# Performance work log

Hardware: AMD Instinct MI355X
Metric: run time of the kernel (lower is better)

Reference implementation:

```python
import jax, jax.numpy as jnp
import numpy as np

B, T, F, C = 16, 750, 4096, 20
R_ACT, R_BKG = 8, 8
KEEP = 0.3  # dropout p=0.7 -> keep prob 0.3, inverted dropout scaling


def setup_inputs() -> dict:
    key = jax.random.key(0)
    k1, k2, k3, k4 = jax.random.split(key, 4)
    x = jax.random.normal(k1, (B, T, F), jnp.float32)
    W_cls = jax.random.normal(k2, (C, F), jnp.float32) * 0.02  # 1x1 conv weight, no bias
    mask_cls = jax.random.bernoulli(k3, KEEP, (B, T, F)).astype(jnp.float32) / KEEP
    select_mask = jax.random.bernoulli(k4, KEEP, (B, T)).astype(jnp.float32) / KEEP
    return {"x": x, "W_cls": W_cls, "mask_cls": mask_cls, "select_mask": select_mask}


def reference(x, W_cls, mask_cls, select_mask):
    features = x  # CAS_Module passes raw input through as 'features'
    # dropout(p=0.7) then 1x1 conv classifier (no bias): (B,T,F)@(F,C)->(B,T,C)
    cas = jnp.einsum('btf,cf->btc', features * mask_cls, W_cls)

    k_act = T // R_ACT
    k_bkg = T // R_BKG

    mag = jnp.linalg.norm(features, axis=2)            # (B,T)
    mag_drop = mag * select_mask                        # dropout-masked magnitudes
    mag_rev = jnp.max(mag, axis=1, keepdims=True) - mag
    mag_rev_drop = mag_rev * select_mask

    _, idx_act = jax.lax.top_k(mag_drop, k_act)         # (B,k_act)
    _, idx_bkg = jax.lax.top_k(mag_rev_drop, k_bkg)     # (B,k_bkg)

    feat_act = jnp.take_along_axis(features, idx_act[:, :, None], axis=1)  # (B,k_act,F)
    feat_bkg = jnp.take_along_axis(features, idx_bkg[:, :, None], axis=1)  # (B,k_bkg,F)

    # per-class top-k over time of cas scores
    topk_scores, _ = jax.lax.top_k(jnp.transpose(cas, (0, 2, 1)), k_act)   # (B,C,k_act)
    score_act = jax.nn.softmax(jnp.mean(topk_scores, axis=2), axis=1)      # (B,C)

    cas_bkg = jnp.take_along_axis(cas, idx_bkg[:, :, None], axis=1)        # (B,k_bkg,C)
    score_bkg = jax.nn.softmax(jnp.mean(cas_bkg, axis=1), axis=1)          # (B,C)

    cas_softmax = jax.nn.softmax(cas, axis=2)                              # (B,T,C)

    return (score_act, score_bkg, feat_act, feat_bkg, features, cas_softmax)
```

## Files before the change

kernel.cpp:

```cpp
#include <hip/hip_runtime.h>

#define BB 16
#define TT 750
#define FF 4096
#define CC 20
#define K_ACT 93
#define K_BKG 93
#define NROWS (BB * TT)

__global__ __launch_bounds__(256) void k_main(
    const float* __restrict__ x, const float* __restrict__ w,
    const float* __restrict__ mask, float* __restrict__ features,
    float* __restrict__ cas_ws, double* __restrict__ mag2_ws)
{
    const int tid = threadIdx.x;
    const int row0 = blockIdx.x * 4;

    float acc[4][CC];
#pragma unroll
    for (int r = 0; r < 4; ++r)
#pragma unroll
        for (int c = 0; c < CC; ++c) acc[r][c] = 0.f;
    double mg[4] = {0.0, 0.0, 0.0, 0.0};

#pragma unroll
    for (int k = 0; k < 2; ++k) {
        const int fb = k * 2048 + tid * 8;
        float mk[4][8];
#pragma unroll
        for (int r = 0; r < 4; ++r) {
            const size_t off = (size_t)(row0 + r) * FF + fb;
            const float4 a0 = *(const float4*)(x + off);
            const float4 a1 = *(const float4*)(x + off + 4);
            const float4 m0 = *(const float4*)(mask + off);
            const float4 m1 = *(const float4*)(mask + off + 4);
            *(float4*)(features + off) = a0;
            *(float4*)(features + off + 4) = a1;
            mk[r][0] = a0.x * m0.x; mk[r][1] = a0.y * m0.y;
            mk[r][2] = a0.z * m0.z; mk[r][3] = a0.w * m0.w;
            mk[r][4] = a1.x * m1.x; mk[r][5] = a1.y * m1.y;
            mk[r][6] = a1.z * m1.z; mk[r][7] = a1.w * m1.w;
            mg[r] = fma((double)a0.x, (double)a0.x, mg[r]);
            mg[r] = fma((double)a0.y, (double)a0.y, mg[r]);
            mg[r] = fma((double)a0.z, (double)a0.z, mg[r]);
            mg[r] = fma((double)a0.w, (double)a0.w, mg[r]);
            mg[r] = fma((double)a1.x, (double)a1.x, mg[r]);
            mg[r] = fma((double)a1.y, (double)a1.y, mg[r]);
            mg[r] = fma((double)a1.z, (double)a1.z, mg[r]);
            mg[r] = fma((double)a1.w, (double)a1.w, mg[r]);
        }
#pragma unroll
        for (int c = 0; c < CC; ++c) {
            const float4 w0 = *(const float4*)(w + (size_t)c * FF + fb);
            const float4 w1 = *(const float4*)(w + (size_t)c * FF + fb + 4);
            float wf[8] = {w0.x, w0.y, w0.z, w0.w, w1.x, w1.y, w1.z, w1.w};
#pragma unroll
            for (int r = 0; r < 4; ++r)
#pragma unroll
                for (int j = 0; j < 8; ++j)
                    acc[r][c] = fmaf(mk[r][j], wf[j], acc[r][c]);
        }
    }

    __shared__ float red[CC][256];
    __shared__ float red2[CC][8];
    __shared__ double dred[256];
    __shared__ double dred2[8];

    for (int r = 0; r < 4; ++r) {
#pragma unroll
        for (int c = 0; c < CC; ++c) red[c][tid] = acc[r][c];
        dred[tid] = mg[r];
        __syncthreads();
        if (tid < 160) {
            const int c = tid >> 3, seg = tid & 7;
            const float4* p = (const float4*)&red[c][seg * 32];
            float s = 0.f;
#pragma unroll
            for (int i = 0; i < 8; ++i) { const float4 v = p[i]; s += (v.x + v.y) + (v.z + v.w); }
            red2[c][seg] = s;
        } else if (tid < 168) {
            const int seg = tid - 160;
            double s = 0.0;
#pragma unroll
            for (int i = 0; i < 32; ++i) s += dred[seg * 32 + i];
            dred2[seg] = s;
        }
        __syncthreads();
        if (tid < CC) {
            float s = 0.f;
#pragma unroll
            for (int i = 0; i < 8; ++i) s += red2[tid][i];
            cas_ws[(size_t)(row0 + r) * CC + tid] = s;
        } else if (tid == CC) {
            double s = 0.0;
#pragma unroll
            for (int i = 0; i < 8; ++i) s += dred2[i];
            mag2_ws[row0 + r] = s;
        }
        __syncthreads();
    }
}

__global__ __launch_bounds__(256) void k_topk(
    const double* __restrict__ mag2_ws, const float* __restrict__ smask,
    int* __restrict__ idxA, int* __restrict__ idxB)
{
    const int b = blockIdx.x;
    const int chunk = blockIdx.y;
    const int tid = threadIdx.x;

    __shared__ double m2[TT];
    __shared__ unsigned char alive[TT];
    __shared__ double mred[256];

    for (int t = tid; t < TT; t += 256) {
        m2[t] = mag2_ws[b * TT + t];
        alive[t] = (smask[b * TT + t] != 0.f);
    }
    __syncthreads();
    double lm = 0.0;
    for (int t = tid; t < TT; t += 256) lm = fmax(lm, m2[t]);
    mred[tid] = lm;
    __syncthreads();
    for (int s = 128; s > 0; s >>= 1) {
        if (tid < s) mred[tid] = fmax(mred[tid], mred[tid + s]);
        __syncthreads();
    }
    const double mx = mred[0];

    const int t = chunk * 250 + tid;
    if (tid < 250 && t < TT && alive[t]) {
        const double v = m2[t];
        const bool posB = v < mx;
        int rA = 0, rB = 0;
        for (int u = 0; u < TT; ++u) {
            if (!alive[u]) continue;
            const double wv = m2[u];
            if (wv > v || (wv == v && u < t)) ++rA;
            if (posB && wv < mx && (wv < v || (wv == v && u < t))) ++rB;
        }
        if (rA < K_ACT) idxA[b * K_ACT + rA] = t;
        if (posB && rB < K_BKG) idxB[b * K_BKG + rB] = t;
    }
}

__global__ __launch_bounds__(256) void k_gather(
    const float* __restrict__ x, const int* __restrict__ idxA,
    const int* __restrict__ idxB, float* __restrict__ featA,
    float* __restrict__ featB)
{
    int g = blockIdx.x;
    const int nA = BB * K_ACT;
    const bool isB = (g >= nA);
    if (isB) g -= nA;
    const int b = g / K_ACT;
    int t = (isB ? idxB : idxA)[g];
    t = min(max(t, 0), TT - 1);
    const float4* src = (const float4*)(x + (size_t)(b * TT + t) * FF);
    float4* dst = (float4*)((isB ? featB : featA) + (size_t)g * FF);
    for (int i = threadIdx.x; i < FF / 4; i += 256) dst[i] = src[i];
}

__global__ __launch_bounds__(256) void k_colmean(
    const float* __restrict__ cas_ws, float* __restrict__ meansA)
{
    const int b = blockIdx.x / CC;
    const int c = blockIdx.x % CC;
    const int tid = threadIdx.x;

    __shared__ float col[TT];
    __shared__ float pred[256];

    for (int t = tid; t < TT; t += 256) col[t] = cas_ws[(size_t)(b * TT + t) * CC + c];
    __syncthreads();

    float loc = 0.f;
    for (int t = tid; t < TT; t += 256) {
        const float v = col[t];
        int cnt = 0;
        for (int u = 0; u < TT; ++u) {
            const float wv = col[u];
            cnt += (wv > v) || (wv == v && u < t);
        }
        if (cnt < K_ACT) loc += v;
    }
    pred[tid] = loc;
    __syncthreads();
    for (int s = 128; s > 0; s >>= 1) {
        if (tid < s) pred[tid] += pred[tid + s];
        __syncthreads();
    }
    if (tid == 0) meansA[b * CC + c] = pred[0] / (float)K_ACT;
}

__global__ void k_scores(
    const float* __restrict__ cas_ws, const float* __restrict__ meansA,
    const int* __restrict__ idxB, float* __restrict__ score_act,
    float* __restrict__ score_bkg)
{
    const int b = blockIdx.x;
    const int tid = threadIdx.x;
    __shared__ float mB[CC];

    if (tid < CC) {
        float s = 0.f;
        for (int j = 0; j < K_BKG; ++j) {
            int t = idxB[b * K_BKG + j];
            t = min(max(t, 0), TT - 1);
            s += cas_ws[(size_t)(b * TT + t) * CC + tid];
        }
        mB[tid] = s / (float)K_BKG;
    }
    __syncthreads();
    if (tid == 0) {
        float va[CC], vb[CC];
        float ma = -1e30f, sa = 0.f;
        for (int c = 0; c < CC; ++c) { va[c] = meansA[b * CC + c]; ma = fmaxf(ma, va[c]); }
        for (int c = 0; c < CC; ++c) { va[c] = expf(va[c] - ma); sa += va[c]; }
        for (int c = 0; c < CC; ++c) score_act[b * CC + c] = va[c] / sa;
        float mb = -1e30f, sb = 0.f;
        for (int c = 0; c < CC; ++c) { vb[c] = mB[c]; mb = fmaxf(mb, vb[c]); }
        for (int c = 0; c < CC; ++c) { vb[c] = expf(vb[c] - mb); sb += vb[c]; }
        for (int c = 0; c < CC; ++c) score_bkg[b * CC + c] = vb[c] / sb;
    }
}

__global__ __launch_bounds__(256) void k_cassm(float* __restrict__ cas)
{
    const int row = blockIdx.x * 256 + threadIdx.x;
    if (row >= NROWS) return;
    float4* p = (float4*)(cas + (size_t)row * CC);
    float v[CC];
#pragma unroll
    for (int i = 0; i < 5; ++i) {
        const float4 q = p[i];
        v[4 * i] = q.x; v[4 * i + 1] = q.y; v[4 * i + 2] = q.z; v[4 * i + 3] = q.w;
    }
    float m = v[0];
#pragma unroll
    for (int c = 1; c < CC; ++c) m = fmaxf(m, v[c]);
    float s = 0.f;
#pragma unroll
    for (int c = 0; c < CC; ++c) { v[c] = expf(v[c] - m); s += v[c]; }
    const float inv = 1.f / s;
#pragma unroll
    for (int i = 0; i < 5; ++i) {
        float4 q;
        q.x = v[4 * i] * inv; q.y = v[4 * i + 1] * inv;
        q.z = v[4 * i + 2] * inv; q.w = v[4 * i + 3] * inv;
        p[i] = q;
    }
}

extern "C" void kernel_launch(void* const* d_in, const int* in_sizes, int n_in,
                              void* d_out, int out_size, void* d_ws, size_t ws_size,
                              hipStream_t stream)
{
    const float* x     = (const float*)d_in[0];
    const float* w     = (const float*)d_in[1];
    const float* mask  = (const float*)d_in[2];
    const float* smask = (const float*)d_in[3];
    float* out = (float*)d_out;

    char* ws = (char*)d_ws;
    double* mag2_ws = (double*)ws;
    int*    idxA    = (int*)(ws + 96000);
    int*    idxB    = (int*)(ws + 101952);
    float*  meansA  = (float*)(ws + 107904);

    float* score_act = out;
    float* score_bkg = out + 320;
    float* featA     = out + 640;
    float* featB     = featA + (size_t)BB * K_ACT * FF;
    float* features  = featB + (size_t)BB * K_BKG * FF;
    float* cas_buf   = features + (size_t)BB * TT * FF;

    k_main<<<NROWS / 4, 256, 0, stream>>>(x, w, mask, features, cas_buf, mag2_ws);
    k_topk<<<dim3(BB, 3), 256, 0, stream>>>(mag2_ws, smask, idxA, idxB);
    k_gather<<<2 * BB * K_ACT, 256, 0, stream>>>(x, idxA, idxB, featA, featB);
    k_colmean<<<BB * CC, 256, 0, stream>>>(cas_buf, meansA);
    k_scores<<<BB, 64, 0, stream>>>(cas_buf, meansA, idxB, score_act, score_bkg);
    k_cassm<<<(NROWS + 255) / 256, 256, 0, stream>>>(cas_buf);
}
```

Baseline: 757.2 us.

## Shrink main tile, use wave-shuffle reductions, nontemporal streams, and merge small kernels

The main kernel now handles 2 rows per block instead of 4 and declares occupancy bounds. Its shared-memory tree reductions are replaced by 64-lane shuffle-xor reductions with a single barrier. The mask loads and feature stores become nontemporal to avoid polluting cache with streamed data. The top-k and column-mean kernels are merged into one launch, as are the gather and score kernels, cutting the launch count from six to four. Halving rows per block means weight vectors are reloaded more often per row, and the many shuffles add ALU work.

New measurement: 1.775 ms. 2.34x slower.

```diff
diff --git a/kernel.cpp b/kernel.cpp
--- a/kernel.cpp
+++ b/kernel.cpp
@@ -8,221 +8,217 @@
 #define K_BKG 93
 #define NROWS (BB * TT)
 
-__global__ __launch_bounds__(256) void k_main(
+typedef float f32x4 __attribute__((ext_vector_type(4)));
+
+__global__ __launch_bounds__(256, 4) void k_main(
     const float* __restrict__ x, const float* __restrict__ w,
     const float* __restrict__ mask, float* __restrict__ features,
     float* __restrict__ cas_ws, double* __restrict__ mag2_ws)
 {
     const int tid = threadIdx.x;
-    const int row0 = blockIdx.x * 4;
-
-    float acc[4][CC];
-#pragma unroll
-    for (int r = 0; r < 4; ++r)
+    const int row0 = blockIdx.x * 2;
+
+    float acc[2][CC];
+#pragma unroll
+    for (int r = 0; r < 2; ++r)
 #pragma unroll
         for (int c = 0; c < CC; ++c) acc[r][c] = 0.f;
-    double mg[4] = {0.0, 0.0, 0.0, 0.0};
+    double mg[2] = {0.0, 0.0};
 
 #pragma unroll
     for (int k = 0; k < 2; ++k) {
         const int fb = k * 2048 + tid * 8;
-        float mk[4][8];
-#pragma unroll
-        for (int r = 0; r < 4; ++r) {
+        float mk[2][8];
+#pragma unroll
+        for (int r = 0; r < 2; ++r) {
             const size_t off = (size_t)(row0 + r) * FF + fb;
-            const float4 a0 = *(const float4*)(x + off);
-            const float4 a1 = *(const float4*)(x + off + 4);
-            const float4 m0 = *(const float4*)(mask + off);
-            const float4 m1 = *(const float4*)(mask + off + 4);
-            *(float4*)(features + off) = a0;
-            *(float4*)(features + off + 4) = a1;
-            mk[r][0] = a0.x * m0.x; mk[r][1] = a0.y * m0.y;
-            mk[r][2] = a0.z * m0.z; mk[r][3] = a0.w * m0.w;
-            mk[r][4] = a1.x * m1.x; mk[r][5] = a1.y * m1.y;
-            mk[r][6] = a1.z * m1.z; mk[r][7] = a1.w * m1.w;
-            mg[r] = fma((double)a0.x, (double)a0.x, mg[r]);
-            mg[r] = fma((double)a0.y, (double)a0.y, mg[r]);
-            mg[r] = fma((double)a0.z, (double)a0.z, mg[r]);
-            mg[r] = fma((double)a0.w, (double)a0.w, mg[r]);
-            mg[r] = fma((double)a1.x, (double)a1.x, mg[r]);
-            mg[r] = fma((double)a1.y, (double)a1.y, mg[r]);
-            mg[r] = fma((double)a1.z, (double)a1.z, mg[r]);
-            mg[r] = fma((double)a1.w, (double)a1.w, mg[r]);
+            const f32x4 a0 = *(const f32x4*)(x + off);
+            const f32x4 a1 = *(const f32x4*)(x + off + 4);
+            const f32x4 m0 = __builtin_nontemporal_load((const f32x4*)(mask + off));
+            const f32x4 m1 = __builtin_nontemporal_load((const f32x4*)(mask + off + 4));
+            __builtin_nontemporal_store(a0, (f32x4*)(features + off));
+            __builtin_nontemporal_store(a1, (f32x4*)(features + off + 4));
+            mk[r][0] = a0[0] * m0[0]; mk[r][1] = a0[1] * m0[1];
+            mk[r][2] = a0[2] * m0[2]; mk[r][3] = a0[3] * m0[3];
+            mk[r][4] = a1[0] * m1[0]; mk[r][5] = a1[1] * m1[1];
+            mk[r][6] = a1[2] * m1[2]; mk[r][7] = a1[3] * m1[3];
+            mg[r] = fma((double)a0[0], (double)a0[0], mg[r]);
+            mg[r] = fma((double)a0[1], (double)a0[1], mg[r]);
+            mg[r] = fma((double)a0[2], (double)a0[2], mg[r]);
+            mg[r] = fma((double)a0[3], (double)a0[3], mg[r]);
+            mg[r] = fma((double)a1[0], (double)a1[0], mg[r]);
+            mg[r] = fma((double)a1[1], (double)a1[1], mg[r]);
+            mg[r] = fma((double)a1[2], (double)a1[2], mg[r]);
+            mg[r] = fma((double)a1[3], (double)a1[3], mg[r]);
         }
 #pragma unroll
         for (int c = 0; c < CC; ++c) {
-            const float4 w0 = *(const float4*)(w + (size_t)c * FF + fb);
-            const float4 w1 = *(const float4*)(w + (size_t)c * FF + fb + 4);
-            float wf[8] = {w0.x, w0.y, w0.z, w0.w, w1.x, w1.y, w1.z, w1.w};
-#pragma unroll
-            for (int r = 0; r < 4; ++r)
+            const f32x4 w0 = *(const f32x4*)(w + (size_t)c * FF + fb);
+            const f32x4 w1 = *(const f32x4*)(w + (size_t)c * FF + fb + 4);
+            float wf[8] = {w0[0], w0[1], w0[2], w0[3], w1[0], w1[1], w1[2], w1[3]};
+#pragma unroll
+            for (int r = 0; r < 2; ++r)
 #pragma unroll
                 for (int j = 0; j < 8; ++j)
                     acc[r][c] = fmaf(mk[r][j], wf[j], acc[r][c]);
         }
     }
 
-    __shared__ float red[CC][256];
-    __shared__ float red2[CC][8];
-    __shared__ double dred[256];
-    __shared__ double dred2[8];
-
-    for (int r = 0; r < 4; ++r) {
-#pragma unroll
-        for (int c = 0; c < CC; ++c) red[c][tid] = acc[r][c];
-        dred[tid] = mg[r];
-        __syncthreads();
-        if (tid < 160) {
-            const int c = tid >> 3, seg = tid & 7;
-            const float4* p = (const float4*)&red[c][seg * 32];
-            float s = 0.f;
-#pragma unroll
-            for (int i = 0; i < 8; ++i) { const float4 v = p[i]; s += (v.x + v.y) + (v.z + v.w); }
-            red2[c][seg] = s;
-        } else if (tid < 168) {
-            const int seg = tid - 160;
-            double s = 0.0;
-#pragma unroll
-            for (int i = 0; i < 32; ++i) s += dred[seg * 32 + i];
-            dred2[seg] = s;
-        }
-        __syncthreads();
+    __shared__ float redw[2][4][CC];
+    __shared__ double redd[2][4];
+    const int wv = tid >> 6;
+    const int ln = tid & 63;
+
+#pragma unroll
+    for (int r = 0; r < 2; ++r) {
+#pragma unroll
+        for (int c = 0; c < CC; ++c) {
+            float v = acc[r][c];
+#pragma unroll
+            for (int off = 1; off < 64; off <<= 1) v += __shfl_xor(v, off, 64);
+            acc[r][c] = v;
+        }
+        double d = mg[r];
+#pragma unroll
+        for (int off = 1; off < 64; off <<= 1) d += __shfl_xor(d, off, 64);
+        if (ln == 0) {
+#pragma unroll
+            for (int c = 0; c < CC; ++c) redw[r][wv][c] = acc[r][c];
+            redd[r][wv] = d;
+        }
+    }
+    __syncthreads();
+    if (tid < 2 * CC) {
+        const int r = tid / CC, c = tid % CC;
+        cas_ws[(size_t)(row0 + r) * CC + c] =
+            (redw[r][0][c] + redw[r][1][c]) + (redw[r][2][c] + redw[r][3][c]);
+    } else if (tid < 2 * CC + 2) {
+        const int r = tid - 2 * CC;
+        mag2_ws[row0 + r] = (redd[r][0] + redd[r][1]) + (redd[r][2] + redd[r][3]);
+    }
+}
+
+__global__ __launch_bounds__(256) void k_mid(
+    const double* __restrict__ mag2_ws, const float* __restrict__ smask,
+    const float* __restrict__ cas_ws,
+    int* __restrict__ idxA, int* __restrict__ idxB, float* __restrict__ meansA)
+{
+    const int bid = blockIdx.x;
+    const int tid = threadIdx.x;
+
+    if (bid < BB * 3) {
+        const int b = bid / 3;
+        const int chunk = bid % 3;
+
+        __shared__ double m2[TT];
+        __shared__ unsigned char alive[TT];
+        __shared__ double mred[256];
+
+        for (int t = tid; t < TT; t += 256) {
+            m2[t] = mag2_ws[b * TT + t];
+            alive[t] = (smask[b * TT + t] != 0.f);
+        }
+        __syncthreads();
+        double lm = 0.0;
+        for (int t = tid; t < TT; t += 256) lm = fmax(lm, m2[t]);
+        mred[tid] = lm;
+        __syncthreads();
+        for (int s = 128; s > 0; s >>= 1) {
+            if (tid < s) mred[tid] = fmax(mred[tid], mred[tid + s]);
+            __syncthreads();
+        }
+        const double mx = mred[0];
+
+        const int t = chunk * 250 + tid;
+        if (tid < 250 && t < TT && alive[t]) {
+            const double v = m2[t];
+            const bool posB = v < mx;
+            int rA = 0, rB = 0;
+            for (int u = 0; u < TT; ++u) {
+                if (!alive[u]) continue;
+                const double wv = m2[u];
+                if (wv > v || (wv == v && u < t)) ++rA;
+                if (posB && wv < mx && (wv < v || (wv == v && u < t))) ++rB;
+            }
+            if (rA < K_ACT) idxA[b * K_ACT + rA] = t;
+            if (posB && rB < K_BKG) idxB[b * K_BKG + rB] = t;
+        }
+    } else {
+        const int cb = bid - BB * 3;
+        const int b = cb / CC;
+        const int c = cb % CC;
+
+        __shared__ float col[TT];
+        __shared__ float pred[256];
+
+        for (int t = tid; t < TT; t += 256) col[t] = cas_ws[(size_t)(b * TT + t) * CC + c];
+        __syncthreads();
+
+        float loc = 0.f;
+        for (int t = tid; t < TT; t += 256) {
+            const float v = col[t];
+            int cnt = 0;
+            for (int u = 0; u < TT; ++u) {
+                const float wv = col[u];
+                cnt += (wv > v) || (wv == v && u < t);
+            }
+            if (cnt < K_ACT) loc += v;
+        }
+        pred[tid] = loc;
+        __syncthreads();
+        for (int s = 128; s > 0; s >>= 1) {
+            if (tid < s) pred[tid] += pred[tid + s];
+            __syncthreads();
+        }
+        if (tid == 0) meansA[b * CC + c] = pred[0] / (float)K_ACT;
+    }
+}
+
+__global__ __launch_bounds__(256) void k_fin(
+    const float* __restrict__ x, const float* __restrict__ cas_ws,
+    const float* __restrict__ meansA,
+    const int* __restrict__ idxA, const int* __restrict__ idxB,
+    float* __restrict__ featA, float* __restrict__ featB,
+    float* __restrict__ score_act, float* __restrict__ score_bkg)
+{
+    int g = blockIdx.x;
+    const int tid = threadIdx.x;
+    const int nA = BB * K_ACT;
+
+    if (g < 2 * nA) {
+        const bool isB = (g >= nA);
+        if (isB) g -= nA;
+        const int b = g / K_ACT;
+        int t = (isB ? idxB : idxA)[g];
+        t = min(max(t, 0), TT - 1);
+        const f32x4* src = (const f32x4*)(x + (size_t)(b * TT + t) * FF);
+        f32x4* dst = (f32x4*)((isB ? featB : featA) + (size_t)g * FF);
+        for (int i = tid; i < FF / 4; i += 256) dst[i] = src[i];
+    } else {
+        const int b = g - 2 * nA;
+        __shared__ float mB[CC];
+
         if (tid < CC) {
             float s = 0.f;
-#pragma unroll
-            for (int i = 0; i < 8; ++i) s += red2[tid][i];
-            cas_ws[(size_t)(row0 + r) * CC + tid] = s;
-        } else if (tid == CC) {
-            double s = 0.0;
-#pragma unroll
-            for (int i = 0; i < 8; ++i) s += dred2[i];
-            mag2_ws[row0 + r] = s;
-        }
-        __syncthreads();
-    }
-}
-
-__global__ __launch_bounds__(256) void k_topk(
-    const double* __restrict__ mag2_ws, const float* __restrict__ smask,
-    int* __restrict__ idxA, int* __restrict__ idxB)
-{
-    const int b = blockIdx.x;
-    const int chunk = blockIdx.y;
-    const int tid = threadIdx.x;
-
-    __shared__ double m2[TT];
-    __shared__ unsigned char alive[TT];
-    __shared__ double mred[256];
-
-    for (int t = tid; t < TT; t += 256) {
-        m2[t] = mag2_ws[b * TT + t];
-        alive[t] = (smask[b * TT + t] != 0.f);
-    }
-    __syncthreads();
-    double lm = 0.0;
-    for (int t = tid; t < TT; t += 256) lm = fmax(lm, m2[t]);
-    mred[tid] = lm;
-    __syncthreads();
-    for (int s = 128; s > 0; s >>= 1) {
-        if (tid < s) mred[tid] = fmax(mred[tid], mred[tid + s]);
-        __syncthreads();
-    }
-    const double mx = mred[0];
-
-    const int t = chunk * 250 + tid;
-    if (tid < 250 && t < TT && alive[t]) {
-        const double v = m2[t];
-        const bool posB = v < mx;
-        int rA = 0, rB = 0;
-        for (int u = 0; u < TT; ++u) {
-            if (!alive[u]) continue;
-            const double wv = m2[u];
-            if (wv > v || (wv == v && u < t)) ++rA;
-            if (posB && wv < mx && (wv < v || (wv == v && u < t))) ++rB;
-        }
-        if (rA < K_ACT) idxA[b * K_ACT + rA] = t;
-        if (posB && rB < K_BKG) idxB[b * K_BKG + rB] = t;
-    }
-}
-
-__global__ __launch_bounds__(256) void k_gather(
-    const float* __restrict__ x, const int* __restrict__ idxA,
-    const int* __restrict__ idxB, float* __restrict__ featA,
-    float* __restrict__ featB)
-{
-    int g = blockIdx.x;
-    const int nA = BB * K_ACT;
-    const bool isB = (g >= nA);
-    if (isB) g -= nA;
-    const int b = g / K_ACT;
-    int t = (isB ? idxB : idxA)[g];
-    t = min(max(t, 0), TT - 1);
-    const float4* src = (const float4*)(x + (size_t)(b * TT + t) * FF);
-    float4* dst = (float4*)((isB ? featB : featA) + (size_t)g * FF);
-    for (int i = threadIdx.x; i < FF / 4; i += 256) dst[i] = src[i];
-}
-
-__global__ __launch_bounds__(256) void k_colmean(
-    const float* __restrict__ cas_ws, float* __restrict__ meansA)
-{
-    const int b = blockIdx.x / CC;
-    const int c = blockIdx.x % CC;
-    const int tid = threadIdx.x;
-
-    __shared__ float col[TT];
-    __shared__ float pred[256];
-
-    for (int t = tid; t < TT; t += 256) col[t] = cas_ws[(size_t)(b * TT + t) * CC + c];
-    __syncthreads();
-
-    float loc = 0.f;
-    for (int t = tid; t < TT; t += 256) {
-        const float v = col[t];
-        int cnt = 0;
-        for (int u = 0; u < TT; ++u) {
-            const float wv = col[u];
-            cnt += (wv > v) || (wv == v && u < t);
-        }
-        if (cnt < K_ACT) loc += v;
-    }
-    pred[tid] = loc;
-    __syncthreads();
-    for (int s = 128; s > 0; s >>= 1) {
-        if (tid < s) pred[tid] += pred[tid + s];
-        __syncthreads();
-    }
-    if (tid == 0) meansA[b * CC + c] = pred[0] / (float)K_ACT;
-}
-
-__global__ void k_scores(
-    const float* __restrict__ cas_ws, const float* __restrict__ meansA,
-    const int* __restrict__ idxB, float* __restrict__ score_act,
-    float* __restrict__ score_bkg)
-{
-    const int b = blockIdx.x;
-    const int tid = threadIdx.x;
-    __shared__ float mB[CC];
-
-    if (tid < CC) {
-        float s = 0.f;
-        for (int j = 0; j < K_BKG; ++j) {
-            int t = idxB[b * K_BKG + j];
-            t = min(max(t, 0), TT - 1);
-            s += cas_ws[(size_t)(b * TT + t) * CC + tid];
-        }
-        mB[tid] = s / (float)K_BKG;
-    }
-    __syncthreads();
-    if (tid == 0) {
-        float va[CC], vb[CC];
-        float ma = -1e30f, sa = 0.f;
-        for (int c = 0; c < CC; ++c) { va[c] = meansA[b * CC + c]; ma = fmaxf(ma, va[c]); }
-        for (int c = 0; c < CC; ++c) { va[c] = expf(va[c] - ma); sa += va[c]; }
-        for (int c = 0; c < CC; ++c) score_act[b * CC + c] = va[c] / sa;
-        float mb = -1e30f, sb = 0.f;
-        for (int c = 0; c < CC; ++c) { vb[c] = mB[c]; mb = fmaxf(mb, vb[c]); }
-        for (int c = 0; c < CC; ++c) { vb[c] = expf(vb[c] - mb); sb += vb[c]; }
-        for (int c = 0; c < CC; ++c) score_bkg[b * CC + c] = vb[c] / sb;
+            for (int j = 0; j < K_BKG; ++j) {
+                int t = idxB[b * K_BKG + j];
+                t = min(max(t, 0), TT - 1);
+                s += cas_ws[(size_t)(b * TT + t) * CC + tid];
+            }
+            mB[tid] = s / (float)K_BKG;
+        }
+        __syncthreads();
+        if (tid == 0) {
+            float va[CC], vb[CC];
+            float ma = -1e30f, sa = 0.f;
+            for (int c = 0; c < CC; ++c) { va[c] = meansA[b * CC + c]; ma = fmaxf(ma, va[c]); }
+            for (int c = 0; c < CC; ++c) { va[c] = expf(va[c] - ma); sa += va[c]; }
+            for (int c = 0; c < CC; ++c) score_act[b * CC + c] = va[c] / sa;
+            float mb = -1e30f, sb = 0.f;
+            for (int c = 0; c < CC; ++c) { vb[c] = mB[c]; mb = fmaxf(mb, vb[c]); }
+            for (int c = 0; c < CC; ++c) { vb[c] = expf(vb[c] - mb); sb += vb[c]; }
+            for (int c = 0; c < CC; ++c) score_bkg[b * CC + c] = vb[c] / sb;
+        }
     }
 }
 
@@ -230,12 +226,12 @@
 {
     const int row = blockIdx.x * 256 + threadIdx.x;
     if (row >= NROWS) return;
-    float4* p = (float4*)(cas + (size_t)row * CC);
+    f32x4* p = (f32x4*)(cas + (size_t)row * CC);
     float v[CC];
 #pragma unroll
     for (int i = 0; i < 5; ++i) {
-        const float4 q = p[i];
-        v[4 * i] = q.x; v[4 * i + 1] = q.y; v[4 * i + 2] = q.z; v[4 * i + 3] = q.w;
+        const f32x4 q = p[i];
+        v[4 * i] = q[0]; v[4 * i + 1] = q[1]; v[4 * i + 2] = q[2]; v[4 * i + 3] = q[3];
     }
     float m = v[0];
 #pragma unroll
@@ -246,9 +242,9 @@
     const float inv = 1.f / s;
 #pragma unroll
     for (int i = 0; i < 5; ++i) {
-        float4 q;
-        q.x = v[4 * i] * inv; q.y = v[4 * i + 1] * inv;
-        q.z = v[4 * i + 2] * inv; q.w = v[4 * i + 3] * inv;
+        f32x4 q;
+        q[0] = v[4 * i] * inv; q[1] = v[4 * i + 1] * inv;
+        q[2] = v[4 * i + 2] * inv; q[3] = v[4 * i + 3] * inv;
         p[i] = q;
     }
 }
@@ -276,10 +272,9 @@
     float* features  = featB + (size_t)BB * K_BKG * FF;
     float* cas_buf   = features + (size_t)BB * TT * FF;
 
-    k_main<<<NROWS / 4, 256, 0, stream>>>(x, w, mask, features, cas_buf, mag2_ws);
-    k_topk<<<dim3(BB, 3), 256, 0, stream>>>(mag2_ws, smask, idxA, idxB);
-    k_gather<<<2 * BB * K_ACT, 256, 0, stream>>>(x, idxA, idxB, featA, featB);
-    k_colmean<<<BB * CC, 256, 0, stream>>>(cas_buf, meansA);
-    k_scores<<<BB, 64, 0, stream>>>(cas_buf, meansA, idxB, score_act, score_bkg);
+    k_main<<<NROWS / 2, 256, 0, stream>>>(x, w, mask, features, cas_buf, mag2_ws);
+    k_mid<<<BB * 3 + BB * CC, 256, 0, stream>>>(mag2_ws, smask, cas_buf, idxA, idxB, meansA);
+    k_fin<<<2 * BB * K_ACT + BB, 256, 0, stream>>>(x, cas_buf, meansA, idxA, idxB,
+                                                   featA, featB, score_act, score_bkg);
     k_cassm<<<(NROWS + 255) / 256, 256, 0, stream>>>(cas_buf);
 }
```
